# Kernel optimization log

Measured on AMD Instinct MI355X. Metric: run time of the kernel, lower is better.

## Reference

```python
import jax, jax.numpy as jnp
import numpy as np

ALPHA = 1.0
EPS = 1e-9
MASK_FILL = 100000.0  # large value pushes masked entries to the end of ascending sort


def setup_inputs() -> dict:
    key = jax.random.key(0)
    k1, k2, k3, k4 = jax.random.split(key, 4)
    bs, nh, n = 128, 32, 2048
    input1 = jax.random.normal(k1, (bs, 4, nh, n), dtype=jnp.float32)
    input2 = jax.random.normal(k2, (bs, 1, nh, n), dtype=jnp.float32)
    mask1 = jax.random.randint(k3, (bs, 4, nh, n), 0, 2).astype(jnp.int32)
    mask2 = jax.random.randint(k4, (bs, 1, nh, n), 0, 2).astype(jnp.int32)
    return {"input1": input1, "mask1": mask1, "input2": input2, "mask2": mask2}


def reference(input1, mask1, input2, mask2):
    # input1: (bs, 4, nh, n) scores; input2/mask2: (bs, 1, nh, n) targets/mask.
    # mask1 is unused by the original forward.
    i2 = jnp.where(mask2 > 0, input2, jnp.float32(MASK_FILL))
    idx = jnp.argsort(i2, axis=-1)                                  # (bs, 1, nh, n)
    mask_sorted = jnp.take_along_axis(mask2, idx, axis=-1).astype(jnp.float32)
    idx4 = jnp.broadcast_to(idx, input1.shape)                      # repeat over the 4 choices
    inputs_sorted = jnp.take_along_axis(input1, idx4, axis=-1)      # (bs, 4, nh, n)
    proj = jnp.exp(ALPHA * inputs_sorted) * mask_sorted             # mode='exp'
    proj_cum = jnp.cumsum(proj, axis=-1) * mask_sorted
    prob = jnp.prod((proj + EPS) / (proj_cum + EPS), axis=-1)       # (bs, 4, nh)
    return jnp.transpose(prob, (0, 2, 1))                           # (bs, nh, 4)
```

## Files before the change

kernel.cpp:

```cpp
#include <hip/hip_runtime.h>

#define N   2048
#define NT  128
#define EPK 16

typedef unsigned int u32;

__device__ __forceinline__ u32 fkey(float f) {
  u32 u = __float_as_uint(f);
  return (u & 0x80000000u) ? ~u : (u | 0x80000000u);
}

__device__ __forceinline__ u32 umin32(u32 a, u32 b) { return a < b ? a : b; }
__device__ __forceinline__ u32 umax32(u32 a, u32 b) { return a < b ? b : a; }

template <int D>
__device__ __forceinline__ u32 exch(u32 x, int lane) {
  if constexpr (D == 1) {
    return (u32)__builtin_amdgcn_update_dpp((int)x, (int)x, 0xB1, 0xF, 0xF, true);
  } else if constexpr (D == 2) {
    return (u32)__builtin_amdgcn_update_dpp((int)x, (int)x, 0x4E, 0xF, 0xF, true);
  } else if constexpr (D == 4) {
    return (u32)__builtin_amdgcn_ds_swizzle((int)x, 0x101F);
  } else if constexpr (D == 8) {
    return (u32)__builtin_amdgcn_update_dpp((int)x, (int)x, 0x128, 0xF, 0xF, true);
  } else if constexpr (D == 16) {
    return (u32)__builtin_amdgcn_ds_swizzle((int)x, 0x401F);
  } else {
    int a = (int)x, b = (int)x;
    asm("v_permlane32_swap_b32 %0, %1" : "+v"(a), "+v"(b));
    return (lane & 32) ? (u32)a : (u32)b;
  }
}

template <int D>
__device__ __forceinline__ void sh_pass(u32* kv, bool keep_min, int lane) {
#pragma unroll
  for (int m = 0; m < EPK; ++m) {
    u32 o = exch<D>(kv[m], lane);
    u32 mn = umin32(kv[m], o), mx = umax32(kv[m], o);
    kv[m] = keep_min ? mn : mx;
  }
}

#define INPASS(J, UPEXPR)                               \
  {                                                     \
    _Pragma("unroll")                                   \
    for (int m = 0; m < EPK; ++m)                       \
      if ((m & (J)) == 0) {                             \
        const bool up_ = (UPEXPR);                      \
        u32 x = kv[m], y = kv[m | (J)];                 \
        u32 mn = umin32(x, y), mx = umax32(x, y);       \
        kv[m] = up_ ? mn : mx;                          \
        kv[m | (J)] = up_ ? mx : mn;                    \
      }                                                 \
  }

__global__ __launch_bounds__(NT, 4) void listmle_kernel(
    const float* __restrict__ input1,
    const float* __restrict__ input2,
    const int* __restrict__ mask2,
    float* __restrict__ out) {
  __shared__ __align__(16) float rows[N];
  __shared__ float hand[2];

  const int tid = threadIdx.x;
  const int lane = tid & 63;
  const int w = tid >> 6;
  const int p = blockIdx.x;
  const int b = p >> 5, h = p & 31;

  u32* keys = (u32*)rows;
  {
    const float4* i2v = (const float4*)(input2 + (size_t)p * N);
    const int4* m2v = (const int4*)(mask2 + (size_t)p * N);
#pragma unroll
    for (int q = 0; q < 4; ++q) {
      float4 vv = i2v[tid + 128 * q];
      int4 mm = m2v[tid + 128 * q];
      const u32 i0 = 4u * (u32)(tid + 128 * q);
      float vs[4] = {vv.x, vv.y, vv.z, vv.w};
      int ms[4] = {mm.x, mm.y, mm.z, mm.w};
#pragma unroll
      for (int r = 0; r < 4; ++r) {
        u32 idx = i0 + r;
        u32 key = (ms[r] > 0) ? ((fkey(vs[r]) & 0xFFFFF800u) | idx)
                              : (0xFFFFF800u | idx);
        keys[idx ^ ((idx >> 5) & 31u)] = key;
      }
    }
  }

  float4 pf[4];
  {
    const float4* r1 = (const float4*)(input1 + ((size_t)((b * 4 + 0) * 32 + h)) * N);
#pragma unroll
    for (int q = 0; q < 4; ++q) pf[q] = r1[tid + 128 * q];
  }

  __syncthreads();
  u32 kv[EPK];
#pragma unroll
  for (int m = 0; m < EPK; ++m) {
    u32 idx = (u32)(w * 1024 + lane * EPK + m);
    kv[m] = keys[idx ^ ((idx >> 5) & 31u)];
  }

  INPASS(1, (m & 2) == 0)
  INPASS(2, (m & 4) == 0) INPASS(1, (m & 4) == 0)
  INPASS(4, (m & 8) == 0) INPASS(2, (m & 8) == 0) INPASS(1, (m & 8) == 0)
  {
    const bool up = (lane & 1) == 0;
    INPASS(8, up) INPASS(4, up) INPASS(2, up) INPASS(1, up)
  }
  {
    const bool up = (lane & 2) == 0;
    sh_pass<1>(kv, ((lane & 1) == 0) == up, lane);
    INPASS(8, up) INPASS(4, up) INPASS(2, up) INPASS(1, up)
  }
  {
    const bool up = (lane & 4) == 0;
    sh_pass<2>(kv, ((lane & 2) == 0) == up, lane);
    sh_pass<1>(kv, ((lane & 1) == 0) == up, lane);
    INPASS(8, up) INPASS(4, up) INPASS(2, up) INPASS(1, up)
  }
  {
    const bool up = (lane & 8) == 0;
    sh_pass<4>(kv, ((lane & 4) == 0) == up, lane);
    sh_pass<2>(kv, ((lane & 2) == 0) == up, lane);
    sh_pass<1>(kv, ((lane & 1) == 0) == up, lane);
    INPASS(8, up) INPASS(4, up) INPASS(2, up) INPASS(1, up)
  }
  {
    const bool up = (lane & 16) == 0;
    sh_pass<8>(kv, ((lane & 8) == 0) == up, lane);
    sh_pass<4>(kv, ((lane & 4) == 0) == up, lane);
    sh_pass<2>(kv, ((lane & 2) == 0) == up, lane);
    sh_pass<1>(kv, ((lane & 1) == 0) == up, lane);
    INPASS(8, up) INPASS(4, up) INPASS(2, up) INPASS(1, up)
  }
  {
    const bool up = (lane & 32) == 0;
    sh_pass<16>(kv, ((lane & 16) == 0) == up, lane);
    sh_pass<8>(kv, ((lane & 8) == 0) == up, lane);
    sh_pass<4>(kv, ((lane & 4) == 0) == up, lane);
    sh_pass<2>(kv, ((lane & 2) == 0) == up, lane);
    sh_pass<1>(kv, ((lane & 1) == 0) == up, lane);
    INPASS(8, up) INPASS(4, up) INPASS(2, up) INPASS(1, up)
  }
  {
    const bool up = (w == 0);
    sh_pass<32>(kv, ((lane & 32) == 0) == up, lane);
    sh_pass<16>(kv, ((lane & 16) == 0) == up, lane);
    sh_pass<8>(kv, ((lane & 8) == 0) == up, lane);
    sh_pass<4>(kv, ((lane & 4) == 0) == up, lane);
    sh_pass<2>(kv, ((lane & 2) == 0) == up, lane);
    sh_pass<1>(kv, ((lane & 1) == 0) == up, lane);
    INPASS(8, up) INPASS(4, up) INPASS(2, up) INPASS(1, up)
  }
  {
    u32* ex = (u32*)rows;
    __syncthreads();
#pragma unroll
    for (int m = 0; m < EPK; ++m) ex[w * 1024 + m * 64 + lane] = kv[m];
    __syncthreads();
#pragma unroll
    for (int m = 0; m < EPK; ++m) {
      u32 o = ex[(w ^ 1) * 1024 + m * 64 + lane];
      kv[m] = (w == 0) ? umin32(kv[m], o) : umax32(kv[m], o);
    }
    __syncthreads();
    sh_pass<32>(kv, (lane & 32) == 0, lane);
    sh_pass<16>(kv, (lane & 16) == 0, lane);
    sh_pass<8>(kv, (lane & 8) == 0, lane);
    sh_pass<4>(kv, (lane & 4) == 0, lane);
    sh_pass<2>(kv, (lane & 2) == 0, lane);
    sh_pass<1>(kv, (lane & 1) == 0, lane);
    INPASS(8, true) INPASS(4, true) INPASS(2, true) INPASS(1, true)
  }

  u32 pk[EPK / 2];
#pragma unroll
  for (int t = 0; t < EPK / 2; ++t) {
    u32 a = kv[2 * t], b2 = kv[2 * t + 1];
    u32 ia = (a & 0x7FFu) | ((a < 0xFFFFF800u) ? 0x800u : 0u);
    u32 ib = (b2 & 0x7FFu) | ((b2 < 0xFFFFF800u) ? 0x800u : 0u);
    pk[t] = ia | (ib << 16);
  }

  for (int c = 0; c < 4; ++c) {
#pragma unroll
    for (int q = 0; q < 4; ++q) ((float4*)rows)[tid + 128 * q] = pf[q];
    __syncthreads();
    if (c < 3) {
      const float4* r1 =
          (const float4*)(input1 + ((size_t)((b * 4 + c + 1) * 32 + h)) * N);
#pragma unroll
      for (int q = 0; q < 4; ++q) pf[q] = r1[tid + 128 * q];
    }

    float e[EPK];
    float lsum = 0.f;
#pragma unroll
    for (int m = 0; m < EPK; ++m) {
      u32 info = (pk[m >> 1] >> ((m & 1) * 16)) & 0xFFFFu;
      float v = rows[info & 0x7FFu];
      float pe = (info & 0x800u) ? __expf(v) : 0.f;
      e[m] = pe;
      lsum += pe;
    }

    float inc = lsum;
#pragma unroll
    for (int d = 1; d < 64; d <<= 1) {
      float o = __shfl_up(inc, d, 64);
      if (lane >= d) inc += o;
    }
    float excl = inc - lsum;

    if (w == 0) {
      float cum = excl;
      float prod = 1.f;
#pragma unroll
      for (int m = 0; m < EPK; ++m) {
        cum += e[m];
        u32 info = pk[m >> 1] >> ((m & 1) * 16);
        if (info & 0x800u) prod *= __fdividef(e[m] + 1e-9f, cum + 1e-9f);
      }
#pragma unroll
      for (int d = 1; d < 64; d <<= 1) prod *= __shfl_xor(prod, d, 64);
      if (lane == 63) hand[0] = inc;
      if (lane == 0) hand[1] = prod;
    }
    __syncthreads();
    if (w == 1) {
      float cum = hand[0] + excl;
      float prod = 1.f;
#pragma unroll
      for (int m = 0; m < EPK; ++m) {
        cum += e[m];
        u32 info = pk[m >> 1] >> ((m & 1) * 16);
        if (info & 0x800u) prod *= __fdividef(e[m] + 1e-9f, cum + 1e-9f);
      }
#pragma unroll
      for (int d = 1; d < 64; d <<= 1) prod *= __shfl_xor(prod, d, 64);
      if (lane == 0) out[(size_t)p * 4 + c] = hand[1] * prod;
    }
  }
}

extern "C" void kernel_launch(void* const* d_in, const int* in_sizes, int n_in,
                              void* d_out, int out_size, void* d_ws, size_t ws_size,
                              hipStream_t stream) {
  const float* input1 = (const float*)d_in[0];
  const float* input2 = (const float*)d_in[2];
  const int* mask2 = (const int*)d_in[3];
  float* out = (float*)d_out;

  const int problems = 128 * 32;
  listmle_kernel<<<problems, NT, 0, stream>>>(input1, input2, mask2, out);
}
```

Baseline: 77.82 us.

## Stage input1 rows directly into double-buffered LDS with async global_load_lds

Replaces register-staged prefetch of each input1 row with `__builtin_amdgcn_global_load_lds` transfers straight into shared memory. Two LDS buffers alternate: the key slab is reused as the second row buffer once the sort finishes. The mid-iteration barrier now waits only on LDS counters, so the in-flight global prefetch is not drained. This removes 16 staging VGPRs and a shared-memory store pass per row. In exchange it doubles LDS use, drops the min-blocks launch hint, and depends on the loop-top `__syncthreads` waiting for the async loads to land.

```diff
diff --git a/kernel.cpp b/kernel.cpp
--- a/kernel.cpp
+++ b/kernel.cpp
@@ -56,12 +56,25 @@
       }                                                 \
   }
 
-__global__ __launch_bounds__(NT, 4) void listmle_kernel(
+__device__ __forceinline__ void stage_row(const float* __restrict__ r1,
+                                          float* buf, int tid, int w) {
+#pragma unroll
+  for (int q = 0; q < 4; ++q) {
+    const float4* src = (const float4*)r1 + (tid + 128 * q);
+    char* dst = (char*)buf + q * 2048 + w * 1024;
+    __builtin_amdgcn_global_load_lds(
+        (const __attribute__((address_space(1))) unsigned int*)src,
+        (__attribute__((address_space(3))) unsigned int*)dst, 16, 0, 0);
+  }
+}
+
+__global__ __launch_bounds__(NT) void listmle_kernel(
     const float* __restrict__ input1,
     const float* __restrict__ input2,
     const int* __restrict__ mask2,
     float* __restrict__ out) {
-  __shared__ __align__(16) float rows[N];
+  __shared__ __align__(16) float rowbuf[N];
+  __shared__ __align__(16) u32 slab[N];
   __shared__ float hand[2];
 
   const int tid = threadIdx.x;
@@ -70,7 +83,6 @@
   const int p = blockIdx.x;
   const int b = p >> 5, h = p & 31;
 
-  u32* keys = (u32*)rows;
   {
     const float4* i2v = (const float4*)(input2 + (size_t)p * N);
     const int4* m2v = (const int4*)(mask2 + (size_t)p * N);
@@ -86,25 +98,19 @@
         u32 idx = i0 + r;
         u32 key = (ms[r] > 0) ? ((fkey(vs[r]) & 0xFFFFF800u) | idx)
                               : (0xFFFFF800u | idx);
-        keys[idx ^ ((idx >> 5) & 31u)] = key;
+        slab[idx ^ ((idx >> 5) & 31u)] = key;
       }
     }
   }
-
-  float4 pf[4];
-  {
-    const float4* r1 = (const float4*)(input1 + ((size_t)((b * 4 + 0) * 32 + h)) * N);
-#pragma unroll
-    for (int q = 0; q < 4; ++q) pf[q] = r1[tid + 128 * q];
-  }
-
   __syncthreads();
   u32 kv[EPK];
 #pragma unroll
   for (int m = 0; m < EPK; ++m) {
     u32 idx = (u32)(w * 1024 + lane * EPK + m);
-    kv[m] = keys[idx ^ ((idx >> 5) & 31u)];
-  }
+    kv[m] = slab[idx ^ ((idx >> 5) & 31u)];
+  }
+
+  stage_row(input1 + ((size_t)((b * 4 + 0) * 32 + h)) * N, rowbuf, tid, w);
 
   INPASS(1, (m & 2) == 0)
   INPASS(2, (m & 4) == 0) INPASS(1, (m & 4) == 0)
@@ -159,14 +165,13 @@
     INPASS(8, up) INPASS(4, up) INPASS(2, up) INPASS(1, up)
   }
   {
-    u32* ex = (u32*)rows;
-    __syncthreads();
-#pragma unroll
-    for (int m = 0; m < EPK; ++m) ex[w * 1024 + m * 64 + lane] = kv[m];
+    __syncthreads();
+#pragma unroll
+    for (int m = 0; m < EPK; ++m) slab[w * 1024 + m * 64 + lane] = kv[m];
     __syncthreads();
 #pragma unroll
     for (int m = 0; m < EPK; ++m) {
-      u32 o = ex[(w ^ 1) * 1024 + m * 64 + lane];
+      u32 o = slab[(w ^ 1) * 1024 + m * 64 + lane];
       kv[m] = (w == 0) ? umin32(kv[m], o) : umax32(kv[m], o);
     }
     __syncthreads();
@@ -188,15 +193,13 @@
     pk[t] = ia | (ib << 16);
   }
 
+#pragma unroll
   for (int c = 0; c < 4; ++c) {
-#pragma unroll
-    for (int q = 0; q < 4; ++q) ((float4*)rows)[tid + 128 * q] = pf[q];
+    float* buf = (c & 1) ? (float*)slab : rowbuf;
     __syncthreads();
     if (c < 3) {
-      const float4* r1 =
-          (const float4*)(input1 + ((size_t)((b * 4 + c + 1) * 32 + h)) * N);
-#pragma unroll
-      for (int q = 0; q < 4; ++q) pf[q] = r1[tid + 128 * q];
+      float* nbuf = (c & 1) ? rowbuf : (float*)slab;
+      stage_row(input1 + ((size_t)((b * 4 + c + 1) * 32 + h)) * N, nbuf, tid, w);
     }
 
     float e[EPK];
@@ -204,7 +207,7 @@
 #pragma unroll
     for (int m = 0; m < EPK; ++m) {
       u32 info = (pk[m >> 1] >> ((m & 1) * 16)) & 0xFFFFu;
-      float v = rows[info & 0x7FFu];
+      float v = buf[info & 0x7FFu];
       float pe = (info & 0x800u) ? __expf(v) : 0.f;
       e[m] = pe;
       lsum += pe;
@@ -232,7 +235,9 @@
       if (lane == 63) hand[0] = inc;
       if (lane == 0) hand[1] = prod;
     }
-    __syncthreads();
+    asm volatile("s_waitcnt lgkmcnt(0)" ::: "memory");
+    __builtin_amdgcn_s_barrier();
+    asm volatile("" ::: "memory");
     if (w == 1) {
       float cum = hand[0] + excl;
       float prod = 1.f;
```

After: 80.67 us. 1.04x slower.
